# Kernel tuning notes

Measured on AMD Instinct MI355X. Metric: run time of the kernel, lower is better.

The kernel has to match this reference:

```python
import jax, jax.numpy as jnp
import numpy as np

G = 60            # 60x60 macroblock MV grid (960px / 16px blocks)
IMAGE_SIZE = 960.0
LN_EPS = 1e-5


def layer_norm(x, g, b):
    mu = jnp.mean(x, -1, keepdims=True)
    var = jnp.var(x, -1, keepdims=True)
    return (x - mu) / jnp.sqrt(var + LN_EPS) * g + b


def setup_inputs() -> dict:
    key = jax.random.key(0)
    ks = iter(jax.random.split(key, 40))
    nk = lambda: next(ks)
    N = 4096
    MVF, BED, H = 64, 32, 128
    D_IN = MVF + BED  # 96

    def lin(out_d, in_d):
        w = jax.random.normal(nk(), (out_d, in_d), jnp.float32) * np.float32(1.0 / np.sqrt(in_d))
        b = jnp.zeros((out_d,), jnp.float32)
        return w, b

    motion_vectors = jax.random.normal(nk(), (1, 2, G, G), jnp.float32)
    xy = jax.random.uniform(nk(), (N, 2), jnp.float32, 0.0, 800.0)
    wh = jax.random.uniform(nk(), (N, 2), jnp.float32, 16.0, 160.0)
    boxes = jnp.concatenate([xy, jnp.clip(xy + wh, 0.0, IMAGE_SIZE)], axis=-1)

    inp = {"motion_vectors": motion_vectors, "boxes": boxes}
    # stats projection: 6 stats (mean/std/range x 2 channels) -> MVF
    inp["W_stats"], inp["b_stats"] = lin(MVF, 6)
    inp["g_stats"] = jnp.ones((MVF,), jnp.float32); inp["be_stats"] = jnp.zeros((MVF,), jnp.float32)
    # box coordinate encoder
    inp["W_b1"], inp["b_b1"] = lin(BED, 4)
    inp["g_b1"] = jnp.ones((BED,), jnp.float32); inp["be_b1"] = jnp.zeros((BED,), jnp.float32)
    inp["W_b2"], inp["b_b2"] = lin(BED, BED)
    inp["g_b2"] = jnp.ones((BED,), jnp.float32); inp["be_b2"] = jnp.zeros((BED,), jnp.float32)
    # single-layer LSTM (torch gate order i,f,g,o)
    inp["W_ih"] = jax.random.normal(nk(), (4 * H, D_IN), jnp.float32) * np.float32(1.0 / np.sqrt(D_IN))
    inp["W_hh"] = jax.random.normal(nk(), (4 * H, H), jnp.float32) * np.float32(1.0 / np.sqrt(H))
    inp["b_ih"] = jnp.zeros((4 * H,), jnp.float32)
    inp["b_hh"] = jnp.zeros((4 * H,), jnp.float32)
    # heads
    inp["W_p1"], inp["b_p1"] = lin(H // 2, H); inp["W_p2"], inp["b_p2"] = lin(2, H // 2)
    inp["W_s1"], inp["b_s1"] = lin(H // 2, H); inp["W_s2"], inp["b_s2"] = lin(2, H // 2)
    inp["W_c1"], inp["b_c1"] = lin(H // 2, H); inp["W_c2"], inp["b_c2"] = lin(1, H // 2)
    return inp


def _box_motion_stats(motion_vectors, boxes_norm):
    # motion_vectors: [1,2,G,G]; boxes_norm: [N,4] in [0,1]
    mvf = motion_vectors[0].reshape(2, G * G)  # [2, 3600]
    x1 = jnp.clip(jnp.floor(boxes_norm[:, 0] * G).astype(jnp.int32), 0, G - 1)
    y1 = jnp.clip(jnp.floor(boxes_norm[:, 1] * G).astype(jnp.int32), 0, G - 1)
    x2 = jnp.clip(jnp.ceil(boxes_norm[:, 2] * G).astype(jnp.int32), x1 + 1, G)
    y2 = jnp.clip(jnp.ceil(boxes_norm[:, 3] * G).astype(jnp.int32), y1 + 1, G)
    idx = jnp.arange(G)
    mx = (idx[None, :] >= x1[:, None]) & (idx[None, :] < x2[:, None])  # [N,G]
    my = (idx[None, :] >= y1[:, None]) & (idx[None, :] < y2[:, None])  # [N,G]
    mask = (my[:, :, None] & mx[:, None, :]).reshape(-1, G * G).astype(mvf.dtype)  # [N,3600]
    cnt = mask.sum(-1, keepdims=True)  # >= 1 by construction
    s = jnp.einsum('nc,kc->nk', mask, mvf)          # [N,2]
    sq = jnp.einsum('nc,kc->nk', mask, mvf * mvf)   # [N,2]
    mean = s / cnt
    std = jnp.sqrt(jnp.clip(sq / cnt - mean * mean, 0.0))
    big = jnp.asarray(1e30, mvf.dtype)
    hi = jnp.where(mask[:, None, :] > 0, mvf[None], -big).max(-1)  # [N,2]
    lo = jnp.where(mask[:, None, :] > 0, mvf[None], big).min(-1)   # [N,2]
    return jnp.concatenate([mean, std, hi - lo], axis=-1)  # [N,6]


def reference(motion_vectors, boxes,
              W_stats, b_stats, g_stats, be_stats,
              W_b1, b_b1, g_b1, be_b1, W_b2, b_b2, g_b2, be_b2,
              W_ih, W_hh, b_ih, b_hh,
              W_p1, b_p1, W_p2, b_p2, W_s1, b_s1, W_s2, b_s2, W_c1, b_c1, W_c2, b_c2):
    N = boxes.shape[0]
    H = W_hh.shape[1]
    boxes_norm = jnp.clip(boxes / IMAGE_SIZE, 0.0, 1.0)

    # per-box motion feature (BoxAlignedMotionEncoder: gather region -> mean/std/range -> proj)
    stats = _box_motion_stats(motion_vectors, boxes_norm)
    mv_feat = jax.nn.relu(layer_norm(stats @ W_stats.T + b_stats, g_stats, be_stats))  # [N,64]

    # box coordinate encoder (dropout = identity in eval)
    h1 = jax.nn.relu(layer_norm(boxes_norm @ W_b1.T + b_b1, g_b1, be_b1))
    box_feat = jax.nn.relu(layer_norm(h1 @ W_b2.T + b_b2, g_b2, be_b2))  # [N,32]

    x = jnp.concatenate([mv_feat, box_feat], axis=-1)  # [N,96]

    # single-step LSTM, zero initial state, torch gate order i,f,g,o
    h0 = jnp.zeros((N, H), x.dtype)
    c0 = jnp.zeros((N, H), x.dtype)
    gates = x @ W_ih.T + h0 @ W_hh.T + b_ih + b_hh
    i, f, g, o = jnp.split(gates, 4, axis=-1)
    c = jax.nn.sigmoid(f) * c0 + jax.nn.sigmoid(i) * jnp.tanh(g)
    h = jax.nn.sigmoid(o) * jnp.tanh(c)  # [N,128]

    pos = jax.nn.relu(h @ W_p1.T + b_p1) @ W_p2.T + b_p2    # [N,2]
    size = jax.nn.relu(h @ W_s1.T + b_s1) @ W_s2.T + b_s2   # [N,2]
    conf = jax.nn.relu(h @ W_c1.T + b_c1) @ W_c2.T + b_c2   # [N,1]
    confidences = jax.nn.sigmoid(conf[:, 0])

    # box update: shift center by deltas, scale w/h by exp(size_deltas)
    x1, y1, x2, y2 = boxes[:, 0], boxes[:, 1], boxes[:, 2], boxes[:, 3]
    cx, cy = (x1 + x2) * 0.5, (y1 + y2) * 0.5
    w, hgt = x2 - x1, y2 - y1
    ncx, ncy = cx + pos[:, 0], cy + pos[:, 1]
    nw, nh = w * jnp.exp(size[:, 0]), hgt * jnp.exp(size[:, 1])
    pred = jnp.stack([ncx - nw * 0.5, ncy - nh * 0.5, ncx + nw * 0.5, ncy + nh * 0.5], axis=-1)
    return jnp.concatenate([pred, confidences[:, None]], axis=-1)  # [N,5]
```

## Files before the change

### kernel.cpp

```cpp
#include <hip/hip_runtime.h>
#include <math.h>

#define GRID_G 60
#define GRID_GG 3600
#define BPB 8

__device__ __forceinline__ float wredsum(float v){
  #pragma unroll
  for (int m = 32; m; m >>= 1) v += __shfl_xor(v, m, 64);
  return v;
}
__device__ __forceinline__ float wredmax(float v){
  #pragma unroll
  for (int m = 32; m; m >>= 1) v = fmaxf(v, __shfl_xor(v, m, 64));
  return v;
}
__device__ __forceinline__ float wredmin(float v){
  #pragma unroll
  for (int m = 32; m; m >>= 1) v = fminf(v, __shfl_xor(v, m, 64));
  return v;
}
__device__ __forceinline__ float frcp(float x){ return __builtin_amdgcn_rcpf(x); }
__device__ __forceinline__ float fsig(float x){ return frcp(1.0f + __expf(-x)); }
__device__ __forceinline__ float ftanh(float x){ return 1.0f - 2.0f*frcp(1.0f + __expf(2.0f*x)); }

__global__ __launch_bounds__(256) void transpose_kernel(
    const float* __restrict__ W_ih,
    const float* __restrict__ W_p1, const float* __restrict__ W_s1,
    const float* __restrict__ W_c1,
    float* __restrict__ wt_ih, float* __restrict__ wt_h)
{
  const int i4 = blockIdx.x * 256 + threadIdx.x;
  if (i4 < 9216) {
    const int e = i4 * 4;
    const int k = e / 384, r0 = e % 384;
    float4 v;
    { const int r = r0;     const int row = (r < 128) ? r : r + 128; v.x = W_ih[row*96 + k]; }
    { const int r = r0 + 1; const int row = (r < 128) ? r : r + 128; v.y = W_ih[row*96 + k]; }
    { const int r = r0 + 2; const int row = (r < 128) ? r : r + 128; v.z = W_ih[row*96 + k]; }
    { const int r = r0 + 3; const int row = (r < 128) ? r : r + 128; v.w = W_ih[row*96 + k]; }
    ((float4*)wt_ih)[i4] = v;
  } else if (i4 < 9216 + 6144) {
    const int j4 = i4 - 9216;
    const int e = j4 * 4;
    const int k = e / 192, r0 = e % 192;
    const float* W = (r0 < 64) ? W_p1 : (r0 < 128) ? W_s1 : W_c1;
    float4 v;
    v.x = W[((r0    ) & 63) * 128 + k];
    v.y = W[((r0 + 1) & 63) * 128 + k];
    v.z = W[((r0 + 2) & 63) * 128 + k];
    v.w = W[((r0 + 3) & 63) * 128 + k];
    ((float4*)wt_h)[j4] = v;
  }
}

__global__ __launch_bounds__(512, 4) void tracker_kernel(
    const float* __restrict__ mv,
    const float* __restrict__ boxes,
    const float* __restrict__ W_stats, const float* __restrict__ b_stats,
    const float* __restrict__ g_stats, const float* __restrict__ be_stats,
    const float* __restrict__ W_b1,  const float* __restrict__ b_b1,
    const float* __restrict__ g_b1,  const float* __restrict__ be_b1,
    const float* __restrict__ W_b2,  const float* __restrict__ b_b2,
    const float* __restrict__ g_b2,  const float* __restrict__ be_b2,
    const float* __restrict__ wt_ih,
    const float* __restrict__ b_ih,  const float* __restrict__ b_hh,
    const float* __restrict__ wt_h,
    const float* __restrict__ b_p1,  const float* __restrict__ W_p2, const float* __restrict__ b_p2,
    const float* __restrict__ b_s1,  const float* __restrict__ W_s2, const float* __restrict__ b_s2,
    const float* __restrict__ b_c1,  const float* __restrict__ W_c2, const float* __restrict__ b_c2,
    float* __restrict__ out, int N)
{
  __shared__ __align__(16) float x_lds[BPB][96];
  __shared__ __align__(16) float sP[4][BPB][384];
  __shared__ __align__(16) float h_lds[BPB][128];
  __shared__ __align__(16) float h1_lds[BPB][32];
  __shared__ float u_lds[3*BPB][65];
  __shared__ float res_lds[BPB][5];

  const int tid  = threadIdx.x;
  const int base = blockIdx.x * BPB;

  {
    const int b    = tid >> 6;
    const int lane = tid & 63;
    const int l32  = lane & 31;
    int gb = base + b; if (gb >= N) gb = N - 1;
    const float4 bx = ((const float4*)boxes)[gb];
    const float bn0 = fminf(fmaxf(bx.x * (1.0f/960.0f), 0.f), 1.f);
    const float bn1 = fminf(fmaxf(bx.y * (1.0f/960.0f), 0.f), 1.f);
    const float bn2 = fminf(fmaxf(bx.z * (1.0f/960.0f), 0.f), 1.f);
    const float bn3 = fminf(fmaxf(bx.w * (1.0f/960.0f), 0.f), 1.f);

    int x1 = (int)floorf(bn0 * 60.f); x1 = min(max(x1, 0), 59);
    int y1 = (int)floorf(bn1 * 60.f); y1 = min(max(y1, 0), 59);
    int x2 = (int)ceilf (bn2 * 60.f); x2 = min(max(x2, x1 + 1), 60);
    int y2 = (int)ceilf (bn3 * 60.f); y2 = min(max(y2, y1 + 1), 60);
    const int w = x2 - x1, hh = y2 - y1;
    const int cnt = w * hh;
    const float rw = 1.0f / (float)w;

    float s0=0.f, s1=0.f, q0=0.f, q1=0.f;
    float hi0=-1e30f, hi1=-1e30f, lo0=1e30f, lo1=1e30f;
    for (int c = lane; c < cnt; c += 64) {
      const int yy = (int)(((float)c + 0.5f) * rw);
      const int xx = c - yy * w;
      const int idx = (y1 + yy) * GRID_G + (x1 + xx);
      const float m0 = mv[idx];
      const float m1 = mv[GRID_GG + idx];
      s0 += m0; q0 += m0*m0; hi0 = fmaxf(hi0, m0); lo0 = fminf(lo0, m0);
      s1 += m1; q1 += m1*m1; hi1 = fmaxf(hi1, m1); lo1 = fminf(lo1, m1);
    }
    s0 = wredsum(s0); q0 = wredsum(q0); hi0 = wredmax(hi0); lo0 = wredmin(lo0);
    s1 = wredsum(s1); q1 = wredsum(q1); hi1 = wredmax(hi1); lo1 = wredmin(lo1);
    const float inv = frcp((float)cnt);
    float st[6];
    st[0] = s0 * inv;
    st[1] = s1 * inv;
    st[2] = sqrtf(fmaxf(q0 * inv - st[0]*st[0], 0.f));
    st[3] = sqrtf(fmaxf(q1 * inv - st[1]*st[1], 0.f));
    st[4] = hi0 - lo0;
    st[5] = hi1 - lo1;

    {
      const float* Wr = W_stats + lane * 6;
      float v = b_stats[lane];
      #pragma unroll
      for (int k = 0; k < 6; ++k) v = fmaf(st[k], Wr[k], v);
      const float mu  = wredsum(v)   * (1.0f/64.0f);
      const float var = wredsum(v*v) * (1.0f/64.0f) - mu*mu;
      x_lds[b][lane] = fmaxf((v - mu) * rsqrtf(var + 1e-5f) * g_stats[lane] + be_stats[lane], 0.f);
    }

    {
      const float* Wr = W_b1 + l32 * 4;
      const float v = b_b1[l32] + bn0*Wr[0] + bn1*Wr[1] + bn2*Wr[2] + bn3*Wr[3];
      const float cv  = (lane < 32) ? v   : 0.f;
      const float cq  = (lane < 32) ? v*v : 0.f;
      const float mu  = wredsum(cv) * (1.0f/32.0f);
      const float var = wredsum(cq) * (1.0f/32.0f) - mu*mu;
      const float h1v = fmaxf((v - mu) * rsqrtf(var + 1e-5f) * g_b1[l32] + be_b1[l32], 0.f);
      if (lane < 32) h1_lds[b][l32] = h1v;
    }
    __threadfence_block();

    {
      const float* Wr = W_b2 + l32 * 32;
      float v = b_b2[l32];
      #pragma unroll
      for (int kk = 0; kk < 8; ++kk) {
        const float4 hv = *(const float4*)(&h1_lds[b][kk * 4]);
        const float4 wv = *(const float4*)(&Wr[kk * 4]);
        v = fmaf(wv.x,hv.x, fmaf(wv.y,hv.y, fmaf(wv.z,hv.z, fmaf(wv.w,hv.w, v))));
      }
      const float cv  = (lane < 32) ? v   : 0.f;
      const float cq  = (lane < 32) ? v*v : 0.f;
      const float mu  = wredsum(cv) * (1.0f/32.0f);
      const float var = wredsum(cq) * (1.0f/32.0f) - mu*mu;
      const float y = fmaxf((v - mu) * rsqrtf(var + 1e-5f) * g_b2[l32] + be_b2[l32], 0.f);
      if (lane < 32) x_lds[b][64 + l32] = y;
    }
  }
  __syncthreads();

  if (tid < 384) {
    const int q = tid % 96;
    const int s = tid / 96;
    const int k0 = s * 24;
    float acc[4][BPB];
    #pragma unroll
    for (int j = 0; j < 4; ++j)
      #pragma unroll
      for (int b = 0; b < BPB; ++b) acc[j][b] = 0.f;
    const float4* WT = (const float4*)wt_ih;
    #pragma unroll 2
    for (int k4 = 0; k4 < 6; ++k4) {
      const int kb = k0 + 4*k4;
      const float4 wv0 = WT[(size_t)(kb    ) * 96 + q];
      const float4 wv1 = WT[(size_t)(kb + 1) * 96 + q];
      const float4 wv2 = WT[(size_t)(kb + 2) * 96 + q];
      const float4 wv3 = WT[(size_t)(kb + 3) * 96 + q];
      #pragma unroll
      for (int b = 0; b < BPB; ++b) {
        const float4 xv = *(const float4*)(&x_lds[b][kb]);
        acc[0][b] = fmaf(wv0.x, xv.x, fmaf(wv1.x, xv.y, fmaf(wv2.x, xv.z, fmaf(wv3.x, xv.w, acc[0][b]))));
        acc[1][b] = fmaf(wv0.y, xv.x, fmaf(wv1.y, xv.y, fmaf(wv2.y, xv.z, fmaf(wv3.y, xv.w, acc[1][b]))));
        acc[2][b] = fmaf(wv0.z, xv.x, fmaf(wv1.z, xv.y, fmaf(wv2.z, xv.z, fmaf(wv3.z, xv.w, acc[2][b]))));
        acc[3][b] = fmaf(wv0.w, xv.x, fmaf(wv1.w, xv.y, fmaf(wv2.w, xv.z, fmaf(wv3.w, xv.w, acc[3][b]))));
      }
    }
    #pragma unroll
    for (int b = 0; b < BPB; ++b) {
      float4 v; v.x = acc[0][b]; v.y = acc[1][b]; v.z = acc[2][b]; v.w = acc[3][b];
      *(float4*)(&sP[s][b][4*q]) = v;
    }
  }
  __syncthreads();

  {
    const int j  = tid & 127;
    const int g2 = tid >> 7;
    const float bi = b_ih[j      ] + b_hh[j      ];
    const float bg = b_ih[j + 256] + b_hh[j + 256];
    const float bo = b_ih[j + 384] + b_hh[j + 384];
    #pragma unroll
    for (int bb = 0; bb < 2; ++bb) {
      const int b = g2 * 2 + bb;
      const float ai = sP[0][b][j      ] + sP[1][b][j      ] + sP[2][b][j      ] + sP[3][b][j      ] + bi;
      const float ag = sP[0][b][128 + j] + sP[1][b][128 + j] + sP[2][b][128 + j] + sP[3][b][128 + j] + bg;
      const float ao = sP[0][b][256 + j] + sP[1][b][256 + j] + sP[2][b][256 + j] + sP[3][b][256 + j] + bo;
      const float c  = fsig(ai) * ftanh(ag);
      h_lds[b][j] = fsig(ao) * ftanh(c);
    }
  }
  __syncthreads();

  if (tid < 384) {
    const int q48 = tid % 48;
    const int s8  = tid / 48;
    const int k0  = s8 * 16;
    float acc[4][BPB];
    #pragma unroll
    for (int j = 0; j < 4; ++j)
      #pragma unroll
      for (int b = 0; b < BPB; ++b) acc[j][b] = 0.f;
    const float4* WT = (const float4*)wt_h;
    #pragma unroll 2
    for (int k4 = 0; k4 < 4; ++k4) {
      const int kb = k0 + 4*k4;
      const float4 wv0 = WT[(size_t)(kb    ) * 48 + q48];
      const float4 wv1 = WT[(size_t)(kb + 1) * 48 + q48];
      const float4 wv2 = WT[(size_t)(kb + 2) * 48 + q48];
      const float4 wv3 = WT[(size_t)(kb + 3) * 48 + q48];
      #pragma unroll
      for (int b = 0; b < BPB; ++b) {
        const float4 hv = *(const float4*)(&h_lds[b][kb]);
        acc[0][b] = fmaf(wv0.x, hv.x, fmaf(wv1.x, hv.y, fmaf(wv2.x, hv.z, fmaf(wv3.x, hv.w, acc[0][b]))));
        acc[1][b] = fmaf(wv0.y, hv.x, fmaf(wv1.y, hv.y, fmaf(wv2.y, hv.z, fmaf(wv3.y, hv.w, acc[1][b]))));
        acc[2][b] = fmaf(wv0.z, hv.x, fmaf(wv1.z, hv.y, fmaf(wv2.z, hv.z, fmaf(wv3.z, hv.w, acc[2][b]))));
        acc[3][b] = fmaf(wv0.w, hv.x, fmaf(wv1.w, hv.y, fmaf(wv2.w, hv.z, fmaf(wv3.w, hv.w, acc[3][b]))));
      }
    }
    const int buf = s8 >> 1;
    const int off = (s8 & 1) * 192;
    #pragma unroll
    for (int b = 0; b < BPB; ++b) {
      float4 v; v.x = acc[0][b]; v.y = acc[1][b]; v.z = acc[2][b]; v.w = acc[3][b];
      *(float4*)(&sP[buf][b][off + 4 * q48]) = v;
    }
  }
  __syncthreads();

  {
    #pragma unroll
    for (int i = 0; i < 3; ++i) {
      const int idx = tid + 512 * i;
      const int b = idx / 192;
      const int r = idx - b * 192;
      const int head = r >> 6, brow = r & 63;
      const float bias = ((head == 0) ? b_p1 : (head == 1) ? b_s1 : b_c1)[brow];
      float v = bias;
      #pragma unroll
      for (int p = 0; p < 8; ++p) v += sP[p >> 1][b][(p & 1) * 192 + r];
      u_lds[head * BPB + b][brow] = fmaxf(v, 0.f);
    }
  }
  __syncthreads();

  if (tid < BPB * 5) {
    const int b = tid / 5, o = tid % 5;
    const int head = (o < 2) ? 0 : (o < 4) ? 1 : 2;
    const float* W2; float bias;
    if      (o == 0) { W2 = W_p2;      bias = b_p2[0]; }
    else if (o == 1) { W2 = W_p2 + 64; bias = b_p2[1]; }
    else if (o == 2) { W2 = W_s2;      bias = b_s2[0]; }
    else if (o == 3) { W2 = W_s2 + 64; bias = b_s2[1]; }
    else             { W2 = W_c2;      bias = b_c2[0]; }
    const float* ur = u_lds[head * BPB + b];
    float a0 = bias, a1 = 0.f, a2 = 0.f, a3 = 0.f;
    #pragma unroll 4
    for (int k = 0; k < 64; k += 4) {
      a0 = fmaf(ur[k  ], W2[k  ], a0);
      a1 = fmaf(ur[k+1], W2[k+1], a1);
      a2 = fmaf(ur[k+2], W2[k+2], a2);
      a3 = fmaf(ur[k+3], W2[k+3], a3);
    }
    res_lds[b][o] = (a0 + a1) + (a2 + a3);
  }
  __syncthreads();

  if (tid < BPB) {
    const int gb = base + tid;
    if (gb < N) {
      const float4 bx = ((const float4*)boxes)[gb];
      const float cx = (bx.x + bx.z) * 0.5f;
      const float cy = (bx.y + bx.w) * 0.5f;
      const float w  = bx.z - bx.x;
      const float hh = bx.w - bx.y;
      const float ncx = cx + res_lds[tid][0];
      const float ncy = cy + res_lds[tid][1];
      const float nw  = w  * __expf(res_lds[tid][2]);
      const float nh  = hh * __expf(res_lds[tid][3]);
      const float cf  = fsig(res_lds[tid][4]);
      float* op = out + (size_t)gb * 5;
      op[0] = ncx - nw * 0.5f;
      op[1] = ncy - nh * 0.5f;
      op[2] = ncx + nw * 0.5f;
      op[3] = ncy + nh * 0.5f;
      op[4] = cf;
    }
  }
}

extern "C" void kernel_launch(void* const* d_in, const int* in_sizes, int n_in,
                              void* d_out, int out_size, void* d_ws, size_t ws_size,
                              hipStream_t stream) {
  (void)n_in; (void)out_size; (void)ws_size;
  const float* mv       = (const float*)d_in[0];
  const float* boxes    = (const float*)d_in[1];
  const float* W_stats  = (const float*)d_in[2];
  const float* b_stats  = (const float*)d_in[3];
  const float* g_stats  = (const float*)d_in[4];
  const float* be_stats = (const float*)d_in[5];
  const float* W_b1     = (const float*)d_in[6];
  const float* b_b1     = (const float*)d_in[7];
  const float* g_b1     = (const float*)d_in[8];
  const float* be_b1    = (const float*)d_in[9];
  const float* W_b2     = (const float*)d_in[10];
  const float* b_b2     = (const float*)d_in[11];
  const float* g_b2     = (const float*)d_in[12];
  const float* be_b2    = (const float*)d_in[13];
  const float* W_ih     = (const float*)d_in[14];
  const float* b_ih     = (const float*)d_in[16];
  const float* b_hh     = (const float*)d_in[17];
  const float* W_p1     = (const float*)d_in[18];
  const float* b_p1     = (const float*)d_in[19];
  const float* W_p2     = (const float*)d_in[20];
  const float* b_p2     = (const float*)d_in[21];
  const float* W_s1     = (const float*)d_in[22];
  const float* b_s1     = (const float*)d_in[23];
  const float* W_s2     = (const float*)d_in[24];
  const float* b_s2     = (const float*)d_in[25];
  const float* W_c1     = (const float*)d_in[26];
  const float* b_c1     = (const float*)d_in[27];
  const float* W_c2     = (const float*)d_in[28];
  const float* b_c2     = (const float*)d_in[29];

  float* wt_ih = (float*)d_ws;
  float* wt_h  = wt_ih + 96 * 384;

  transpose_kernel<<<60, 256, 0, stream>>>(W_ih, W_p1, W_s1, W_c1, wt_ih, wt_h);

  const int N = in_sizes[1] / 4;
  const int grid = (N + BPB - 1) / BPB;
  tracker_kernel<<<grid, 512, 0, stream>>>(
      mv, boxes,
      W_stats, b_stats, g_stats, be_stats,
      W_b1, b_b1, g_b1, be_b1,
      W_b2, b_b2, g_b2, be_b2,
      wt_ih, b_ih, b_hh,
      wt_h,
      b_p1, W_p2, b_p2,
      b_s1, W_s2, b_s2,
      b_c1, W_c2, b_c2,
      (float*)d_out, N);
}
```

Before: 134.9 us.

## Keep LSTM and head weights in registers, process two box groups per block

Drops the separate transpose kernel. Each thread now loads its slice of W_ih and the head first-layer weights straight from the original row-major layout into registers once. The block then loops over two groups of 8 boxes, so those weights are reused and the grid is halved. This removes a kernel launch and the repeated weight loads from global memory. The cost is much higher register pressure (about 160 floats of weights per thread) with the occupancy hint dropped, which may lower occupancy or cause spills.

```diff
diff --git a/kernel.cpp b/kernel.cpp
--- a/kernel.cpp
+++ b/kernel.cpp
@@ -3,7 +3,6 @@
 
 #define GRID_G 60
 #define GRID_GG 3600
-#define BPB 8
 
 __device__ __forceinline__ float wredsum(float v){
   #pragma unroll
@@ -24,37 +23,7 @@
 __device__ __forceinline__ float fsig(float x){ return frcp(1.0f + __expf(-x)); }
 __device__ __forceinline__ float ftanh(float x){ return 1.0f - 2.0f*frcp(1.0f + __expf(2.0f*x)); }
 
-__global__ __launch_bounds__(256) void transpose_kernel(
-    const float* __restrict__ W_ih,
-    const float* __restrict__ W_p1, const float* __restrict__ W_s1,
-    const float* __restrict__ W_c1,
-    float* __restrict__ wt_ih, float* __restrict__ wt_h)
-{
-  const int i4 = blockIdx.x * 256 + threadIdx.x;
-  if (i4 < 9216) {
-    const int e = i4 * 4;
-    const int k = e / 384, r0 = e % 384;
-    float4 v;
-    { const int r = r0;     const int row = (r < 128) ? r : r + 128; v.x = W_ih[row*96 + k]; }
-    { const int r = r0 + 1; const int row = (r < 128) ? r : r + 128; v.y = W_ih[row*96 + k]; }
-    { const int r = r0 + 2; const int row = (r < 128) ? r : r + 128; v.z = W_ih[row*96 + k]; }
-    { const int r = r0 + 3; const int row = (r < 128) ? r : r + 128; v.w = W_ih[row*96 + k]; }
-    ((float4*)wt_ih)[i4] = v;
-  } else if (i4 < 9216 + 6144) {
-    const int j4 = i4 - 9216;
-    const int e = j4 * 4;
-    const int k = e / 192, r0 = e % 192;
-    const float* W = (r0 < 64) ? W_p1 : (r0 < 128) ? W_s1 : W_c1;
-    float4 v;
-    v.x = W[((r0    ) & 63) * 128 + k];
-    v.y = W[((r0 + 1) & 63) * 128 + k];
-    v.z = W[((r0 + 2) & 63) * 128 + k];
-    v.w = W[((r0 + 3) & 63) * 128 + k];
-    ((float4*)wt_h)[j4] = v;
-  }
-}
-
-__global__ __launch_bounds__(512, 4) void tracker_kernel(
+__global__ __launch_bounds__(512) void tracker_kernel(
     const float* __restrict__ mv,
     const float* __restrict__ boxes,
     const float* __restrict__ W_stats, const float* __restrict__ b_stats,
@@ -63,259 +32,277 @@
     const float* __restrict__ g_b1,  const float* __restrict__ be_b1,
     const float* __restrict__ W_b2,  const float* __restrict__ b_b2,
     const float* __restrict__ g_b2,  const float* __restrict__ be_b2,
-    const float* __restrict__ wt_ih,
-    const float* __restrict__ b_ih,  const float* __restrict__ b_hh,
-    const float* __restrict__ wt_h,
-    const float* __restrict__ b_p1,  const float* __restrict__ W_p2, const float* __restrict__ b_p2,
-    const float* __restrict__ b_s1,  const float* __restrict__ W_s2, const float* __restrict__ b_s2,
-    const float* __restrict__ b_c1,  const float* __restrict__ W_c2, const float* __restrict__ b_c2,
+    const float* __restrict__ W_ih,  const float* __restrict__ b_ih,
+    const float* __restrict__ b_hh,
+    const float* __restrict__ W_p1,  const float* __restrict__ b_p1,
+    const float* __restrict__ W_p2,  const float* __restrict__ b_p2,
+    const float* __restrict__ W_s1,  const float* __restrict__ b_s1,
+    const float* __restrict__ W_s2,  const float* __restrict__ b_s2,
+    const float* __restrict__ W_c1,  const float* __restrict__ b_c1,
+    const float* __restrict__ W_c2,  const float* __restrict__ b_c2,
     float* __restrict__ out, int N)
 {
-  __shared__ __align__(16) float x_lds[BPB][96];
-  __shared__ __align__(16) float sP[4][BPB][384];
-  __shared__ __align__(16) float h_lds[BPB][128];
-  __shared__ __align__(16) float h1_lds[BPB][32];
-  __shared__ float u_lds[3*BPB][65];
-  __shared__ float res_lds[BPB][5];
-
-  const int tid  = threadIdx.x;
-  const int base = blockIdx.x * BPB;
-
-  {
-    const int b    = tid >> 6;
-    const int lane = tid & 63;
-    const int l32  = lane & 31;
-    int gb = base + b; if (gb >= N) gb = N - 1;
-    const float4 bx = ((const float4*)boxes)[gb];
-    const float bn0 = fminf(fmaxf(bx.x * (1.0f/960.0f), 0.f), 1.f);
-    const float bn1 = fminf(fmaxf(bx.y * (1.0f/960.0f), 0.f), 1.f);
-    const float bn2 = fminf(fmaxf(bx.z * (1.0f/960.0f), 0.f), 1.f);
-    const float bn3 = fminf(fmaxf(bx.w * (1.0f/960.0f), 0.f), 1.f);
-
-    int x1 = (int)floorf(bn0 * 60.f); x1 = min(max(x1, 0), 59);
-    int y1 = (int)floorf(bn1 * 60.f); y1 = min(max(y1, 0), 59);
-    int x2 = (int)ceilf (bn2 * 60.f); x2 = min(max(x2, x1 + 1), 60);
-    int y2 = (int)ceilf (bn3 * 60.f); y2 = min(max(y2, y1 + 1), 60);
-    const int w = x2 - x1, hh = y2 - y1;
-    const int cnt = w * hh;
-    const float rw = 1.0f / (float)w;
-
-    float s0=0.f, s1=0.f, q0=0.f, q1=0.f;
-    float hi0=-1e30f, hi1=-1e30f, lo0=1e30f, lo1=1e30f;
-    for (int c = lane; c < cnt; c += 64) {
-      const int yy = (int)(((float)c + 0.5f) * rw);
-      const int xx = c - yy * w;
-      const int idx = (y1 + yy) * GRID_G + (x1 + xx);
-      const float m0 = mv[idx];
-      const float m1 = mv[GRID_GG + idx];
-      s0 += m0; q0 += m0*m0; hi0 = fmaxf(hi0, m0); lo0 = fminf(lo0, m0);
-      s1 += m1; q1 += m1*m1; hi1 = fmaxf(hi1, m1); lo1 = fminf(lo1, m1);
-    }
-    s0 = wredsum(s0); q0 = wredsum(q0); hi0 = wredmax(hi0); lo0 = wredmin(lo0);
-    s1 = wredsum(s1); q1 = wredsum(q1); hi1 = wredmax(hi1); lo1 = wredmin(lo1);
-    const float inv = frcp((float)cnt);
-    float st[6];
-    st[0] = s0 * inv;
-    st[1] = s1 * inv;
-    st[2] = sqrtf(fmaxf(q0 * inv - st[0]*st[0], 0.f));
-    st[3] = sqrtf(fmaxf(q1 * inv - st[1]*st[1], 0.f));
-    st[4] = hi0 - lo0;
-    st[5] = hi1 - lo1;
+  __shared__ __align__(16) float x_lds[8][96];
+  __shared__ __align__(16) float sP[4][8][384];
+  __shared__ __align__(16) float h_lds[8][128];
+  __shared__ __align__(16) float h1_lds[8][32];
+  __shared__ float u_lds[24][65];
+  __shared__ float res_lds[8][5];
+
+  const int tid = threadIdx.x;
+
+  const int q   = tid % 96;
+  const int s   = tid / 96;
+  const int q48 = tid % 48;
+  const int s8  = tid / 48;
+  float4 w2r[4][6];
+  float4 w3r[4][4];
+  if (tid < 384) {
+    const int k0 = s * 24;
+    #pragma unroll
+    for (int j = 0; j < 4; ++j) {
+      const int rp  = 4*q + j;
+      const int row = (rp < 128) ? rp : rp + 128;
+      const float* src = W_ih + (size_t)row * 96 + k0;
+      #pragma unroll
+      for (int m = 0; m < 6; ++m) w2r[j][m] = *(const float4*)(src + 4*m);
+    }
+    const int k0h = s8 * 16;
+    #pragma unroll
+    for (int j = 0; j < 4; ++j) {
+      const int rpp  = 4*q48 + j;
+      const int head = rpp >> 6;
+      const float* W1 = (head == 0) ? W_p1 : (head == 1) ? W_s1 : W_c1;
+      const float* src = W1 + (size_t)(rpp & 63) * 128 + k0h;
+      #pragma unroll
+      for (int m = 0; m < 4; ++m) w3r[j][m] = *(const float4*)(src + 4*m);
+    }
+  }
+
+  for (int g = 0; g < 2; ++g) {
+    const int base = (blockIdx.x * 2 + g) * 8;
 
     {
-      const float* Wr = W_stats + lane * 6;
-      float v = b_stats[lane];
-      #pragma unroll
-      for (int k = 0; k < 6; ++k) v = fmaf(st[k], Wr[k], v);
-      const float mu  = wredsum(v)   * (1.0f/64.0f);
-      const float var = wredsum(v*v) * (1.0f/64.0f) - mu*mu;
-      x_lds[b][lane] = fmaxf((v - mu) * rsqrtf(var + 1e-5f) * g_stats[lane] + be_stats[lane], 0.f);
-    }
+      const int b    = tid >> 6;
+      const int lane = tid & 63;
+      const int l32  = lane & 31;
+      int gb = base + b; if (gb >= N) gb = N - 1;
+      const float4 bx = ((const float4*)boxes)[gb];
+      const float bn0 = fminf(fmaxf(bx.x * (1.0f/960.0f), 0.f), 1.f);
+      const float bn1 = fminf(fmaxf(bx.y * (1.0f/960.0f), 0.f), 1.f);
+      const float bn2 = fminf(fmaxf(bx.z * (1.0f/960.0f), 0.f), 1.f);
+      const float bn3 = fminf(fmaxf(bx.w * (1.0f/960.0f), 0.f), 1.f);
+
+      int x1 = (int)floorf(bn0 * 60.f); x1 = min(max(x1, 0), 59);
+      int y1 = (int)floorf(bn1 * 60.f); y1 = min(max(y1, 0), 59);
+      int x2 = (int)ceilf (bn2 * 60.f); x2 = min(max(x2, x1 + 1), 60);
+      int y2 = (int)ceilf (bn3 * 60.f); y2 = min(max(y2, y1 + 1), 60);
+      const int w = x2 - x1, hh = y2 - y1;
+      const int cnt = w * hh;
+      const float rw = 1.0f / (float)w;
+
+      float s0=0.f, s1=0.f, q0=0.f, q1=0.f;
+      float hi0=-1e30f, hi1=-1e30f, lo0=1e30f, lo1=1e30f;
+      for (int c = lane; c < cnt; c += 64) {
+        const int yy = (int)(((float)c + 0.5f) * rw);
+        const int xx = c - yy * w;
+        const int idx = (y1 + yy) * GRID_G + (x1 + xx);
+        const float m0 = mv[idx];
+        const float m1 = mv[GRID_GG + idx];
+        s0 += m0; q0 += m0*m0; hi0 = fmaxf(hi0, m0); lo0 = fminf(lo0, m0);
+        s1 += m1; q1 += m1*m1; hi1 = fmaxf(hi1, m1); lo1 = fminf(lo1, m1);
+      }
+      s0 = wredsum(s0); q0 = wredsum(q0); hi0 = wredmax(hi0); lo0 = wredmin(lo0);
+      s1 = wredsum(s1); q1 = wredsum(q1); hi1 = wredmax(hi1); lo1 = wredmin(lo1);
+      const float inv = frcp((float)cnt);
+      float st[6];
+      st[0] = s0 * inv;
+      st[1] = s1 * inv;
+      st[2] = sqrtf(fmaxf(q0 * inv - st[0]*st[0], 0.f));
+      st[3] = sqrtf(fmaxf(q1 * inv - st[1]*st[1], 0.f));
+      st[4] = hi0 - lo0;
+      st[5] = hi1 - lo1;
+
+      {
+        const float* Wr = W_stats + lane * 6;
+        float v = b_stats[lane];
+        #pragma unroll
+        for (int k = 0; k < 6; ++k) v = fmaf(st[k], Wr[k], v);
+        const float mu  = wredsum(v)   * (1.0f/64.0f);
+        const float var = wredsum(v*v) * (1.0f/64.0f) - mu*mu;
+        x_lds[b][lane] = fmaxf((v - mu) * rsqrtf(var + 1e-5f) * g_stats[lane] + be_stats[lane], 0.f);
+      }
+
+      {
+        const float* Wr = W_b1 + l32 * 4;
+        const float v = b_b1[l32] + bn0*Wr[0] + bn1*Wr[1] + bn2*Wr[2] + bn3*Wr[3];
+        const float cv  = (lane < 32) ? v   : 0.f;
+        const float cq  = (lane < 32) ? v*v : 0.f;
+        const float mu  = wredsum(cv) * (1.0f/32.0f);
+        const float var = wredsum(cq) * (1.0f/32.0f) - mu*mu;
+        const float h1v = fmaxf((v - mu) * rsqrtf(var + 1e-5f) * g_b1[l32] + be_b1[l32], 0.f);
+        if (lane < 32) h1_lds[b][l32] = h1v;
+      }
+      __threadfence_block();
+
+      {
+        const float* Wr = W_b2 + l32 * 32;
+        float v = b_b2[l32];
+        #pragma unroll
+        for (int kk = 0; kk < 8; ++kk) {
+          const float4 hv = *(const float4*)(&h1_lds[b][kk * 4]);
+          const float4 wv = *(const float4*)(&Wr[kk * 4]);
+          v = fmaf(wv.x,hv.x, fmaf(wv.y,hv.y, fmaf(wv.z,hv.z, fmaf(wv.w,hv.w, v))));
+        }
+        const float cv  = (lane < 32) ? v   : 0.f;
+        const float cq  = (lane < 32) ? v*v : 0.f;
+        const float mu  = wredsum(cv) * (1.0f/32.0f);
+        const float var = wredsum(cq) * (1.0f/32.0f) - mu*mu;
+        const float y = fmaxf((v - mu) * rsqrtf(var + 1e-5f) * g_b2[l32] + be_b2[l32], 0.f);
+        if (lane < 32) x_lds[b][64 + l32] = y;
+      }
+    }
+    __syncthreads();
+
+    if (tid < 384) {
+      const int k0 = s * 24;
+      float acc[4][8];
+      #pragma unroll
+      for (int j = 0; j < 4; ++j)
+        #pragma unroll
+        for (int b = 0; b < 8; ++b) acc[j][b] = 0.f;
+      #pragma unroll
+      for (int m = 0; m < 6; ++m) {
+        #pragma unroll
+        for (int b = 0; b < 8; ++b) {
+          const float4 xv = *(const float4*)(&x_lds[b][k0 + 4*m]);
+          #pragma unroll
+          for (int j = 0; j < 4; ++j)
+            acc[j][b] = fmaf(w2r[j][m].x, xv.x, fmaf(w2r[j][m].y, xv.y,
+                        fmaf(w2r[j][m].z, xv.z, fmaf(w2r[j][m].w, xv.w, acc[j][b]))));
+        }
+      }
+      #pragma unroll
+      for (int b = 0; b < 8; ++b) {
+        float4 v; v.x = acc[0][b]; v.y = acc[1][b]; v.z = acc[2][b]; v.w = acc[3][b];
+        *(float4*)(&sP[s][b][4*q]) = v;
+      }
+    }
+    __syncthreads();
 
     {
-      const float* Wr = W_b1 + l32 * 4;
-      const float v = b_b1[l32] + bn0*Wr[0] + bn1*Wr[1] + bn2*Wr[2] + bn3*Wr[3];
-      const float cv  = (lane < 32) ? v   : 0.f;
-      const float cq  = (lane < 32) ? v*v : 0.f;
-      const float mu  = wredsum(cv) * (1.0f/32.0f);
-      const float var = wredsum(cq) * (1.0f/32.0f) - mu*mu;
-      const float h1v = fmaxf((v - mu) * rsqrtf(var + 1e-5f) * g_b1[l32] + be_b1[l32], 0.f);
-      if (lane < 32) h1_lds[b][l32] = h1v;
-    }
-    __threadfence_block();
+      const int j  = tid & 127;
+      const int g2 = tid >> 7;
+      const float bi = b_ih[j      ] + b_hh[j      ];
+      const float bg = b_ih[j + 256] + b_hh[j + 256];
+      const float bo = b_ih[j + 384] + b_hh[j + 384];
+      #pragma unroll
+      for (int bb = 0; bb < 2; ++bb) {
+        const int b = g2 * 2 + bb;
+        const float ai = sP[0][b][j      ] + sP[1][b][j      ] + sP[2][b][j      ] + sP[3][b][j      ] + bi;
+        const float ag = sP[0][b][128 + j] + sP[1][b][128 + j] + sP[2][b][128 + j] + sP[3][b][128 + j] + bg;
+        const float ao = sP[0][b][256 + j] + sP[1][b][256 + j] + sP[2][b][256 + j] + sP[3][b][256 + j] + bo;
+        const float c  = fsig(ai) * ftanh(ag);
+        h_lds[b][j] = fsig(ao) * ftanh(c);
+      }
+    }
+    __syncthreads();
+
+    if (tid < 384) {
+      const int k0 = s8 * 16;
+      float acc[4][8];
+      #pragma unroll
+      for (int j = 0; j < 4; ++j)
+        #pragma unroll
+        for (int b = 0; b < 8; ++b) acc[j][b] = 0.f;
+      #pragma unroll
+      for (int m = 0; m < 4; ++m) {
+        #pragma unroll
+        for (int b = 0; b < 8; ++b) {
+          const float4 hv = *(const float4*)(&h_lds[b][k0 + 4*m]);
+          #pragma unroll
+          for (int j = 0; j < 4; ++j)
+            acc[j][b] = fmaf(w3r[j][m].x, hv.x, fmaf(w3r[j][m].y, hv.y,
+                        fmaf(w3r[j][m].z, hv.z, fmaf(w3r[j][m].w, hv.w, acc[j][b]))));
+        }
+      }
+      const int buf = s8 >> 1;
+      const int off = (s8 & 1) * 192;
+      #pragma unroll
+      for (int b = 0; b < 8; ++b) {
+        float4 v; v.x = acc[0][b]; v.y = acc[1][b]; v.z = acc[2][b]; v.w = acc[3][b];
+        *(float4*)(&sP[buf][b][off + 4 * q48]) = v;
+      }
+    }
+    __syncthreads();
 
     {
-      const float* Wr = W_b2 + l32 * 32;
-      float v = b_b2[l32];
-      #pragma unroll
-      for (int kk = 0; kk < 8; ++kk) {
-        const float4 hv = *(const float4*)(&h1_lds[b][kk * 4]);
-        const float4 wv = *(const float4*)(&Wr[kk * 4]);
-        v = fmaf(wv.x,hv.x, fmaf(wv.y,hv.y, fmaf(wv.z,hv.z, fmaf(wv.w,hv.w, v))));
-      }
-      const float cv  = (lane < 32) ? v   : 0.f;
-      const float cq  = (lane < 32) ? v*v : 0.f;
-      const float mu  = wredsum(cv) * (1.0f/32.0f);
-      const float var = wredsum(cq) * (1.0f/32.0f) - mu*mu;
-      const float y = fmaxf((v - mu) * rsqrtf(var + 1e-5f) * g_b2[l32] + be_b2[l32], 0.f);
-      if (lane < 32) x_lds[b][64 + l32] = y;
-    }
-  }
-  __syncthreads();
-
-  if (tid < 384) {
-    const int q = tid % 96;
-    const int s = tid / 96;
-    const int k0 = s * 24;
-    float acc[4][BPB];
-    #pragma unroll
-    for (int j = 0; j < 4; ++j)
-      #pragma unroll
-      for (int b = 0; b < BPB; ++b) acc[j][b] = 0.f;
-    const float4* WT = (const float4*)wt_ih;
-    #pragma unroll 2
-    for (int k4 = 0; k4 < 6; ++k4) {
-      const int kb = k0 + 4*k4;
-      const float4 wv0 = WT[(size_t)(kb    ) * 96 + q];
-      const float4 wv1 = WT[(size_t)(kb + 1) * 96 + q];
-      const float4 wv2 = WT[(size_t)(kb + 2) * 96 + q];
-      const float4 wv3 = WT[(size_t)(kb + 3) * 96 + q];
-      #pragma unroll
-      for (int b = 0; b < BPB; ++b) {
-        const float4 xv = *(const float4*)(&x_lds[b][kb]);
-        acc[0][b] = fmaf(wv0.x, xv.x, fmaf(wv1.x, xv.y, fmaf(wv2.x, xv.z, fmaf(wv3.x, xv.w, acc[0][b]))));
-        acc[1][b] = fmaf(wv0.y, xv.x, fmaf(wv1.y, xv.y, fmaf(wv2.y, xv.z, fmaf(wv3.y, xv.w, acc[1][b]))));
-        acc[2][b] = fmaf(wv0.z, xv.x, fmaf(wv1.z, xv.y, fmaf(wv2.z, xv.z, fmaf(wv3.z, xv.w, acc[2][b]))));
-        acc[3][b] = fmaf(wv0.w, xv.x, fmaf(wv1.w, xv.y, fmaf(wv2.w, xv.z, fmaf(wv3.w, xv.w, acc[3][b]))));
-      }
-    }
-    #pragma unroll
-    for (int b = 0; b < BPB; ++b) {
-      float4 v; v.x = acc[0][b]; v.y = acc[1][b]; v.z = acc[2][b]; v.w = acc[3][b];
-      *(float4*)(&sP[s][b][4*q]) = v;
-    }
-  }
-  __syncthreads();
-
-  {
-    const int j  = tid & 127;
-    const int g2 = tid >> 7;
-    const float bi = b_ih[j      ] + b_hh[j      ];
-    const float bg = b_ih[j + 256] + b_hh[j + 256];
-    const float bo = b_ih[j + 384] + b_hh[j + 384];
-    #pragma unroll
-    for (int bb = 0; bb < 2; ++bb) {
-      const int b = g2 * 2 + bb;
-      const float ai = sP[0][b][j      ] + sP[1][b][j      ] + sP[2][b][j      ] + sP[3][b][j      ] + bi;
-      const float ag = sP[0][b][128 + j] + sP[1][b][128 + j] + sP[2][b][128 + j] + sP[3][b][128 + j] + bg;
-      const float ao = sP[0][b][256 + j] + sP[1][b][256 + j] + sP[2][b][256 + j] + sP[3][b][256 + j] + bo;
-      const float c  = fsig(ai) * ftanh(ag);
-      h_lds[b][j] = fsig(ao) * ftanh(c);
-    }
-  }
-  __syncthreads();
-
-  if (tid < 384) {
-    const int q48 = tid % 48;
-    const int s8  = tid / 48;
-    const int k0  = s8 * 16;
-    float acc[4][BPB];
-    #pragma unroll
-    for (int j = 0; j < 4; ++j)
-      #pragma unroll
-      for (int b = 0; b < BPB; ++b) acc[j][b] = 0.f;
-    const float4* WT = (const float4*)wt_h;
-    #pragma unroll 2
-    for (int k4 = 0; k4 < 4; ++k4) {
-      const int kb = k0 + 4*k4;
-      const float4 wv0 = WT[(size_t)(kb    ) * 48 + q48];
-      const float4 wv1 = WT[(size_t)(kb + 1) * 48 + q48];
-      const float4 wv2 = WT[(size_t)(kb + 2) * 48 + q48];
-      const float4 wv3 = WT[(size_t)(kb + 3) * 48 + q48];
-      #pragma unroll
-      for (int b = 0; b < BPB; ++b) {
-        const float4 hv = *(const float4*)(&h_lds[b][kb]);
-        acc[0][b] = fmaf(wv0.x, hv.x, fmaf(wv1.x, hv.y, fmaf(wv2.x, hv.z, fmaf(wv3.x, hv.w, acc[0][b]))));
-        acc[1][b] = fmaf(wv0.y, hv.x, fmaf(wv1.y, hv.y, fmaf(wv2.y, hv.z, fmaf(wv3.y, hv.w, acc[1][b]))));
-        acc[2][b] = fmaf(wv0.z, hv.x, fmaf(wv1.z, hv.y, fmaf(wv2.z, hv.z, fmaf(wv3.z, hv.w, acc[2][b]))));
-        acc[3][b] = fmaf(wv0.w, hv.x, fmaf(wv1.w, hv.y, fmaf(wv2.w, hv.z, fmaf(wv3.w, hv.w, acc[3][b]))));
-      }
-    }
-    const int buf = s8 >> 1;
-    const int off = (s8 & 1) * 192;
-    #pragma unroll
-    for (int b = 0; b < BPB; ++b) {
-      float4 v; v.x = acc[0][b]; v.y = acc[1][b]; v.z = acc[2][b]; v.w = acc[3][b];
-      *(float4*)(&sP[buf][b][off + 4 * q48]) = v;
-    }
-  }
-  __syncthreads();
-
-  {
-    #pragma unroll
-    for (int i = 0; i < 3; ++i) {
-      const int idx = tid + 512 * i;
-      const int b = idx / 192;
-      const int r = idx - b * 192;
-      const int head = r >> 6, brow = r & 63;
-      const float bias = ((head == 0) ? b_p1 : (head == 1) ? b_s1 : b_c1)[brow];
-      float v = bias;
-      #pragma unroll
-      for (int p = 0; p < 8; ++p) v += sP[p >> 1][b][(p & 1) * 192 + r];
-      u_lds[head * BPB + b][brow] = fmaxf(v, 0.f);
-    }
-  }
-  __syncthreads();
-
-  if (tid < BPB * 5) {
-    const int b = tid / 5, o = tid % 5;
-    const int head = (o < 2) ? 0 : (o < 4) ? 1 : 2;
-    const float* W2; float bias;
-    if      (o == 0) { W2 = W_p2;      bias = b_p2[0]; }
-    else if (o == 1) { W2 = W_p2 + 64; bias = b_p2[1]; }
-    else if (o == 2) { W2 = W_s2;      bias = b_s2[0]; }
-    else if (o == 3) { W2 = W_s2 + 64; bias = b_s2[1]; }
-    else             { W2 = W_c2;      bias = b_c2[0]; }
-    const float* ur = u_lds[head * BPB + b];
-    float a0 = bias, a1 = 0.f, a2 = 0.f, a3 = 0.f;
-    #pragma unroll 4
-    for (int k = 0; k < 64; k += 4) {
-      a0 = fmaf(ur[k  ], W2[k  ], a0);
-      a1 = fmaf(ur[k+1], W2[k+1], a1);
-      a2 = fmaf(ur[k+2], W2[k+2], a2);
-      a3 = fmaf(ur[k+3], W2[k+3], a3);
-    }
-    res_lds[b][o] = (a0 + a1) + (a2 + a3);
-  }
-  __syncthreads();
-
-  if (tid < BPB) {
-    const int gb = base + tid;
-    if (gb < N) {
-      const float4 bx = ((const float4*)boxes)[gb];
-      const float cx = (bx.x + bx.z) * 0.5f;
-      const float cy = (bx.y + bx.w) * 0.5f;
-      const float w  = bx.z - bx.x;
-      const float hh = bx.w - bx.y;
-      const float ncx = cx + res_lds[tid][0];
-      const float ncy = cy + res_lds[tid][1];
-      const float nw  = w  * __expf(res_lds[tid][2]);
-      const float nh  = hh * __expf(res_lds[tid][3]);
-      const float cf  = fsig(res_lds[tid][4]);
-      float* op = out + (size_t)gb * 5;
-      op[0] = ncx - nw * 0.5f;
-      op[1] = ncy - nh * 0.5f;
-      op[2] = ncx + nw * 0.5f;
-      op[3] = ncy + nh * 0.5f;
-      op[4] = cf;
-    }
+      #pragma unroll
+      for (int i = 0; i < 3; ++i) {
+        const int idx = tid + 512 * i;
+        const int b = idx / 192;
+        const int r = idx - b * 192;
+        const int head = r >> 6, brow = r & 63;
+        const float bias = ((head == 0) ? b_p1 : (head == 1) ? b_s1 : b_c1)[brow];
+        float v = bias;
+        #pragma unroll
+        for (int p = 0; p < 8; ++p) v += sP[p >> 1][b][(p & 1) * 192 + r];
+        u_lds[head * 8 + b][brow] = fmaxf(v, 0.f);
+      }
+    }
+    __syncthreads();
+
+    if (tid < 40) {
+      const int b = tid / 5, o = tid % 5;
+      const int head = (o < 2) ? 0 : (o < 4) ? 1 : 2;
+      const float* W2; float bias;
+      if      (o == 0) { W2 = W_p2;      bias = b_p2[0]; }
+      else if (o == 1) { W2 = W_p2 + 64; bias = b_p2[1]; }
+      else if (o == 2) { W2 = W_s2;      bias = b_s2[0]; }
+      else if (o == 3) { W2 = W_s2 + 64; bias = b_s2[1]; }
+      else             { W2 = W_c2;      bias = b_c2[0]; }
+      const float* ur = u_lds[head * 8 + b];
+      float a0 = bias, a1 = 0.f, a2 = 0.f, a3 = 0.f;
+      #pragma unroll 4
+      for (int k = 0; k < 64; k += 4) {
+        a0 = fmaf(ur[k  ], W2[k  ], a0);
+        a1 = fmaf(ur[k+1], W2[k+1], a1);
+        a2 = fmaf(ur[k+2], W2[k+2], a2);
+        a3 = fmaf(ur[k+3], W2[k+3], a3);
+      }
+      res_lds[b][o] = (a0 + a1) + (a2 + a3);
+    }
+    __syncthreads();
+
+    if (tid < 8) {
+      const int gb = base + tid;
+      if (gb < N) {
+        const float4 bx = ((const float4*)boxes)[gb];
+        const float cx = (bx.x + bx.z) * 0.5f;
+        const float cy = (bx.y + bx.w) * 0.5f;
+        const float w  = bx.z - bx.x;
+        const float hh = bx.w - bx.y;
+        const float ncx = cx + res_lds[tid][0];
+        const float ncy = cy + res_lds[tid][1];
+        const float nw  = w  * __expf(res_lds[tid][2]);
+        const float nh  = hh * __expf(res_lds[tid][3]);
+        const float cf  = fsig(res_lds[tid][4]);
+        float* op = out + (size_t)gb * 5;
+        op[0] = ncx - nw * 0.5f;
+        op[1] = ncy - nh * 0.5f;
+        op[2] = ncx + nw * 0.5f;
+        op[3] = ncy + nh * 0.5f;
+        op[4] = cf;
+      }
+    }
+    __syncthreads();
   }
 }
 
 extern "C" void kernel_launch(void* const* d_in, const int* in_sizes, int n_in,
                               void* d_out, int out_size, void* d_ws, size_t ws_size,
                               hipStream_t stream) {
-  (void)n_in; (void)out_size; (void)ws_size;
+  (void)n_in; (void)out_size; (void)d_ws; (void)ws_size;
   const float* mv       = (const float*)d_in[0];
   const float* boxes    = (const float*)d_in[1];
   const float* W_stats  = (const float*)d_in[2];
@@ -346,22 +333,16 @@
   const float* W_c2     = (const float*)d_in[28];
   const float* b_c2     = (const float*)d_in[29];
 
-  float* wt_ih = (float*)d_ws;
-  float* wt_h  = wt_ih + 96 * 384;
-
-  transpose_kernel<<<60, 256, 0, stream>>>(W_ih, W_p1, W_s1, W_c1, wt_ih, wt_h);
-
   const int N = in_sizes[1] / 4;
-  const int grid = (N + BPB - 1) / BPB;
+  const int grid = (N + 15) / 16;
   tracker_kernel<<<grid, 512, 0, stream>>>(
       mv, boxes,
       W_stats, b_stats, g_stats, be_stats,
       W_b1, b_b1, g_b1, be_b1,
       W_b2, b_b2, g_b2, be_b2,
-      wt_ih, b_ih, b_hh,
-      wt_h,
-      b_p1, W_p2, b_p2,
-      b_s1, W_s2, b_s2,
-      b_c1, W_c2, b_c2,
+      W_ih, b_ih, b_hh,
+      W_p1, b_p1, W_p2, b_p2,
+      W_s1, b_s1, W_s2, b_s2,
+      W_c1, b_c1, W_c2, b_c2,
       (float*)d_out, N);
 }
```

After: 183.8 us. 36.3% more time.
